# Performance work log

Hardware: AMD Instinct MI355X
Metric: run time of the kernel (lower is better)

Reference implementation:

```python
import jax, jax.numpy as jnp
import numpy as np

INPUT_SIZE = 695 + 2 * 406 + 84  # 1591
HIDDEN = 1024
NUM_LAYERS = 2
B, T = 8, 2048


def _make_linear(key, fan_in, fan_out, forget_bias):
    kw, kb = jax.random.split(key)
    bound = 1.0 / np.sqrt(fan_in)
    W = jax.random.uniform(kw, (fan_in, fan_out), minval=-bound, maxval=bound, dtype=jnp.float32)
    b = jax.random.uniform(kb, (fan_out,), minval=-bound, maxval=bound, dtype=jnp.float32)
    H = fan_out // 3
    b = b.at[H:2 * H].set(forget_bias)  # init_input_passthrough: forget-gate bias = 6.0
    return W, b


def setup_inputs() -> dict:
    key = jax.random.key(0)
    k1, k2, k3, k4, k5 = jax.random.split(key, 5)
    prev_actions = jax.random.uniform(k1, (B, T, 695), dtype=jnp.float32)
    states = jax.random.uniform(k2, (B, T, 812), dtype=jnp.float32)
    metadata = jax.random.uniform(k3, (B, T, 84), dtype=jnp.float32)
    W1, b1 = _make_linear(k4, INPUT_SIZE, 3 * HIDDEN, 6.0)
    W2, b2 = _make_linear(k5, HIDDEN, 3 * HIDDEN, 6.0)
    return {"prev_actions": prev_actions, "states": states, "metadata": metadata,
            "W1": W1, "b1": b1, "W2": W2, "b2": b2}


def forget_mult(f, z):
    # c_t = f_t * z_t + (1 - f_t) * c_{t-1}, c_0 = 0; parallel (log-depth) scan over time.
    a = 1.0 - f          # decay
    b = f * z            # input term
    def combine(c1, c2):
        a1, b1 = c1
        a2, b2 = c2
        return a1 * a2, a2 * b1 + b2
    _, c = jax.lax.associative_scan(combine, (a, b), axis=-2)
    return c


def qrnn_layer(x, W, b):
    y = jnp.einsum('btd,dh->bth', x, W) + b          # [B,T,3H]
    Z, Fg, O = jnp.split(y, 3, axis=-1)
    C = forget_mult(jax.nn.sigmoid(Fg), jax.nn.relu(Z))  # [B,T,H]
    out = jax.nn.sigmoid(O) * C
    return out, C[..., -1, :]


def reference(prev_actions, states, metadata, W1, b1, W2, b2):
    x = jnp.concatenate([prev_actions, states, metadata], axis=-1)  # [B,T,1591]
    hs = []
    for W, b in ((W1, b1), (W2, b2)):
        x, h_last = qrnn_layer(x, W, b)
        hs.append(h_last)
    h = jnp.stack(hs, axis=-2)  # [B, num_layers, H]
    return x, h
```

## Files before the change

### kernel.cpp

```cpp
#include <hip/hip_runtime.h>

typedef unsigned short u16;
typedef unsigned int   u32;
typedef __attribute__((ext_vector_type(8))) short bf16x8;
typedef __attribute__((ext_vector_type(4))) float f32x4;

#define B_ 8
#define T_ 2048
#define M_ 16384
#define N_ 3072
#define H_ 1024
#define L_ 64
#define NC_ 32

__device__ __forceinline__ u16 f2bf(float f) {
    union { float f; unsigned u; } v; v.f = f;
    unsigned r = v.u + 0x7FFFu + ((v.u >> 16) & 1u);
    return (u16)(r >> 16);
}
__device__ __forceinline__ float bf2f(u16 s) {
    union { unsigned u; float f; } v; v.u = ((unsigned)s) << 16;
    return v.f;
}
__device__ __forceinline__ float sigm(float x) {
    return 1.f / (1.f + __expf(-x));
}

__device__ __forceinline__ void gload_lds16(const void* g, void* l) {
    __builtin_amdgcn_global_load_lds(
        (const __attribute__((address_space(1))) unsigned int*)g,
        (__attribute__((address_space(3))) unsigned int*)l,
        16, 0, 0);
}

__global__ void concat_cast(const float* __restrict__ pa, const float* __restrict__ st,
                            const float* __restrict__ md, u16* __restrict__ x) {
    const int m = blockIdx.x;
    const float* pam = pa + (size_t)m * 695;
    const float* stm = st + (size_t)m * 812;
    const float* mdm = md + (size_t)m * 84;
    u16* xm = x + (size_t)m * 1600;
    for (int d = threadIdx.x; d < 1600; d += 256) {
        float v;
        if (d < 695)       v = pam[d];
        else if (d < 1507) v = stm[d - 695];
        else if (d < 1591) v = mdm[d - 1507];
        else               v = 0.f;
        xm[d] = f2bf(v);
    }
}

__global__ void wtrans(const float* __restrict__ W, u16* __restrict__ Wt, int K, int Kp) {
    __shared__ float tile[32][33];
    const int n0 = blockIdx.x << 5;
    const int k0 = blockIdx.y << 5;
    const int tx = threadIdx.x & 31, ty = threadIdx.x >> 5;
    #pragma unroll
    for (int i = 0; i < 32; i += 8) {
        int k = k0 + ty + i;
        tile[ty + i][tx] = (k < K) ? W[(size_t)k * N_ + n0 + tx] : 0.f;
    }
    __syncthreads();
    #pragma unroll
    for (int i = 0; i < 32; i += 8) {
        int n = n0 + ty + i;
        Wt[(size_t)n * Kp + k0 + tx] = f2bf(tile[tx][ty + i]);
    }
}

#define AO_(c, kh) ((((c) << 2) + (kh)) << 13)
#define BO_(c, kh) ((((c) << 2) + 2 + (kh)) << 13)

__global__ __launch_bounds__(512, 1)
void gemm8p(const u16* __restrict__ A, const u16* __restrict__ Bt,
            const float* __restrict__ bias, u16* __restrict__ Y,
            int Kp, int NK, int NBN) {
    __shared__ u16 lds[65536];
    const int tid = threadIdx.x;
    const int w = tid >> 6, l = tid & 63;
    const int wm = w >> 2, wn = w & 3;

    const int cpx = gridDim.x >> 3;
    const int xg = (blockIdx.x & 7) * cpx + (blockIdx.x >> 3);
    const int bm = xg / NBN, bn = xg % NBN;
    const int brow = bm << 8, bcol = bn << 8;

    const int srow = l >> 2;
    const int gslot = (l & 3) ^ (srow & 3);
    const u16* ga = A  + (size_t)(brow + w * 32 + srow) * Kp + gslot * 8;
    const u16* gb = Bt + (size_t)(bcol + w * 32 + srow) * Kp + gslot * 8;
    const int ldst = w << 10;

    const int fl = ((l & 15) << 5) + ((((l >> 4) ^ (l & 3)) & 3) << 3);
    const int abase0 = (wm << 7) << 5;
    const int bbase0 = (wn << 6) << 5;

#define STG(OFF, gp, kt, kh) do {                                              \
    gload_lds16((gp) + (size_t)(kt) * 64 + (kh) * 32, &lds[(OFF) + ldst]);     \
    gload_lds16((gp) + 16 * (size_t)Kp + (size_t)(kt) * 64 + (kh) * 32,        \
                &lds[(OFF) + ldst + 512]);                                     \
} while (0)

    f32x4 acc[8][4] = {};
    bf16x8 bfr[4];

    STG(AO_(0, 0), ga, 0, 0); STG(BO_(0, 0), gb, 0, 0);
    STG(AO_(0, 1), ga, 0, 1); STG(BO_(0, 1), gb, 0, 1);
    STG(AO_(1, 0), ga, 1, 0); STG(BO_(1, 0), gb, 1, 0);
    asm volatile("s_waitcnt vmcnt(4)" ::: "memory");
    __builtin_amdgcn_s_barrier();
    asm volatile("" ::: "memory");

#define PHASE(CH, KH, LOADB, STAGECODE, VMW) do {                              \
    bf16x8 af[4];                                                              \
    { const int ab = AO_(cur, KH) + abase0 + ((CH) << 11);                     \
      _Pragma("unroll")                                                        \
      for (int mf = 0; mf < 4; ++mf)                                           \
          af[mf] = *reinterpret_cast<const bf16x8*>(&lds[ab + (mf << 9) + fl]);\
    }                                                                          \
    if (LOADB) {                                                               \
        const int bb = BO_(cur, KH) + bbase0;                                  \
        _Pragma("unroll")                                                      \
        for (int nf = 0; nf < 4; ++nf)                                         \
            bfr[nf] = *reinterpret_cast<const bf16x8*>(&lds[bb + (nf << 9) + fl]); \
    }                                                                          \
    STAGECODE;                                                                 \
    if (VMW) asm volatile("s_waitcnt vmcnt(4)" ::: "memory");                  \
    asm volatile("" ::: "memory");                                             \
    __builtin_amdgcn_s_barrier();                                              \
    asm volatile("s_waitcnt lgkmcnt(0)" ::: "memory");                         \
    __builtin_amdgcn_sched_barrier(0);                                         \
    __builtin_amdgcn_s_setprio(1);                                             \
    _Pragma("unroll")                                                          \
    for (int mf = 0; mf < 4; ++mf)                                             \
        _Pragma("unroll")                                                      \
        for (int nf = 0; nf < 4; ++nf)                                         \
            acc[(CH) * 4 + mf][nf] = __builtin_amdgcn_mfma_f32_16x16x32_bf16(  \
                af[mf], bfr[nf], acc[(CH) * 4 + mf][nf], 0, 0, 0);             \
    __builtin_amdgcn_s_setprio(0);                                             \
    __builtin_amdgcn_sched_barrier(0);                                         \
    __builtin_amdgcn_s_barrier();                                              \
    asm volatile("" ::: "memory");                                             \
} while (0)

    for (int kt = 0; kt < NK; ++kt) {
        const int cur = kt & 1;
        const int kn1 = (kt + 1 < NK) ? kt + 1 : kt;
        const int kn2 = (kt + 2 < NK) ? kt + 2 : kt;
        PHASE(0, 0, 1, { STG(AO_(cur ^ 1, 1), ga, kn1, 1); }, 0);
        PHASE(1, 0, 0, { STG(BO_(cur ^ 1, 1), gb, kn1, 1); }, 1);
        PHASE(0, 1, 1, { STG(AO_(cur, 0),     ga, kn2, 0); }, 0);
        PHASE(1, 1, 0, { STG(BO_(cur, 0),     gb, kn2, 0); }, 1);
    }

    asm volatile("s_waitcnt vmcnt(0)" ::: "memory");

    const int crow0 = brow + wm * 128 + ((l >> 4) << 2);
    const int ccol0 = bcol + wn * 64 + (l & 15);
    #pragma unroll
    for (int nf = 0; nf < 4; ++nf) {
        const int gc = ccol0 + nf * 16;
        const float bv = bias[gc];
        #pragma unroll
        for (int mfi = 0; mfi < 8; ++mfi) {
            #pragma unroll
            for (int j = 0; j < 4; ++j)
                Y[(size_t)(crow0 + mfi * 16 + j) * N_ + gc] = f2bf(acc[mfi][nf][j] + bv);
        }
    }
#undef PHASE
#undef STG
}

__global__ void scan_p1(const u16* __restrict__ y, float* __restrict__ aprod,
                        float* __restrict__ cend) {
    const int hb = blockIdx.x & 1;
    const int chunk = (blockIdx.x >> 1) & (NC_ - 1);
    const int b = blockIdx.x >> 6;
    const int h = (hb << 9) + (threadIdx.x << 1);
    const u16* yb = y + ((size_t)b * T_ + (size_t)chunk * L_) * N_;
    float a0 = 1.f, a1 = 1.f, c0 = 0.f, c1 = 0.f;
    #pragma unroll 4
    for (int t = 0; t < L_; ++t) {
        const u32 zz = *reinterpret_cast<const u32*>(&yb[t * N_ + h]);
        const u32 ff = *reinterpret_cast<const u32*>(&yb[t * N_ + H_ + h]);
        const float f0 = sigm(bf2f((u16)ff));
        const float f1 = sigm(bf2f((u16)(ff >> 16)));
        const float z0 = fmaxf(bf2f((u16)zz), 0.f);
        const float z1 = fmaxf(bf2f((u16)(zz >> 16)), 0.f);
        c0 = f0 * z0 + (1.f - f0) * c0;  a0 *= (1.f - f0);
        c1 = f1 * z1 + (1.f - f1) * c1;  a1 *= (1.f - f1);
    }
    const size_t idx = ((size_t)b * NC_ + chunk) * H_ + h;
    *reinterpret_cast<float2*>(&aprod[idx]) = make_float2(a0, a1);
    *reinterpret_cast<float2*>(&cend[idx])  = make_float2(c0, c1);
}

__global__ void scan_p2(const float* __restrict__ aprod, const float* __restrict__ cend,
                        float* __restrict__ cin, float* __restrict__ hout, int layer) {
    const int b = blockIdx.x >> 2;
    const int h = ((blockIdx.x & 3) << 8) + threadIdx.x;
    float c = 0.f;
    #pragma unroll
    for (int k = 0; k < NC_; ++k) {
        const size_t idx = ((size_t)b * NC_ + k) * H_ + h;
        cin[idx] = c;
        c = aprod[idx] * c + cend[idx];
    }
    hout[(size_t)(((b << 1) + layer) << 10) + h] = c;
}

__global__ void scan_p3(const u16* __restrict__ y, const float* __restrict__ cin,
                        void* __restrict__ xout, int layer) {
    const int hb = blockIdx.x & 1;
    const int chunk = (blockIdx.x >> 1) & (NC_ - 1);
    const int b = blockIdx.x >> 6;
    const int h = (hb << 9) + (threadIdx.x << 1);
    const u16* yb = y + ((size_t)b * T_ + (size_t)chunk * L_) * N_;
    const size_t cidx = ((size_t)b * NC_ + chunk) * H_ + h;
    const float2 cv = *reinterpret_cast<const float2*>(&cin[cidx]);
    float c0 = cv.x, c1 = cv.y;
    u32*    xo_bf = (u32*)xout;
    float2* xo_f  = (float2*)xout;
    const size_t obase = ((size_t)b * T_ + (size_t)chunk * L_) * H_ + h;
    #pragma unroll 4
    for (int t = 0; t < L_; ++t) {
        const u32 zz = *reinterpret_cast<const u32*>(&yb[t * N_ + h]);
        const u32 ff = *reinterpret_cast<const u32*>(&yb[t * N_ + H_ + h]);
        const u32 oo = *reinterpret_cast<const u32*>(&yb[t * N_ + 2 * H_ + h]);
        const float f0 = sigm(bf2f((u16)ff));
        const float f1 = sigm(bf2f((u16)(ff >> 16)));
        const float z0 = fmaxf(bf2f((u16)zz), 0.f);
        const float z1 = fmaxf(bf2f((u16)(zz >> 16)), 0.f);
        c0 = f0 * z0 + (1.f - f0) * c0;
        c1 = f1 * z1 + (1.f - f1) * c1;
        const float o0 = sigm(bf2f((u16)oo)) * c0;
        const float o1 = sigm(bf2f((u16)(oo >> 16))) * c1;
        const size_t oi = obase + (size_t)t * H_;
        if (layer) xo_f[oi >> 1] = make_float2(o0, o1);
        else       xo_bf[oi >> 1] = (u32)f2bf(o0) | ((u32)f2bf(o1) << 16);
    }
}

extern "C" void kernel_launch(void* const* d_in, const int* in_sizes, int n_in,
                              void* d_out, int out_size, void* d_ws, size_t ws_size,
                              hipStream_t stream) {
    const float* pa = (const float*)d_in[0];
    const float* st = (const float*)d_in[1];
    const float* md = (const float*)d_in[2];
    const float* W1 = (const float*)d_in[3];
    const float* b1 = (const float*)d_in[4];
    const float* W2 = (const float*)d_in[5];
    const float* b2 = (const float*)d_in[6];
    float* out = (float*)d_out;

    char* ws = (char*)d_ws;
    const size_t y_bytes = (size_t)M_ * N_ * 2;
    const size_t x_bytes = (size_t)M_ * 1600 * 2;
    u16* y  = (u16*)ws;
    u16* x  = (u16*)(ws + y_bytes);
    u16* Wt = (u16*)(ws + y_bytes + x_bytes);
    char* scr = ws + y_bytes + (size_t)M_ * H_ * 2;
    const size_t sarr = (size_t)B_ * NC_ * H_ * 4;
    float* aprod = (float*)scr;
    float* cend  = (float*)(scr + sarr);
    float* cin   = (float*)(scr + 2 * sarr);

    float* hout = out + (size_t)M_ * H_;

    const int grid_g = (M_ / 256) * (N_ / 256);

    concat_cast<<<M_, 256, 0, stream>>>(pa, st, md, x);
    wtrans<<<dim3(N_ / 32, 50), 256, 0, stream>>>(W1, Wt, 1591, 1600);
    gemm8p<<<grid_g, 512, 0, stream>>>(x, Wt, b1, y, 1600, 25, N_ / 256);
    scan_p1<<<B_ * NC_ * 2, 256, 0, stream>>>(y, aprod, cend);
    scan_p2<<<32, 256, 0, stream>>>(aprod, cend, cin, hout, 0);
    scan_p3<<<B_ * NC_ * 2, 256, 0, stream>>>(y, cin, x, 0);

    wtrans<<<dim3(N_ / 32, 32), 256, 0, stream>>>(W2, Wt, 1024, 1024);
    gemm8p<<<grid_g, 512, 0, stream>>>(x, Wt, b2, y, 1024, 16, N_ / 256);
    scan_p1<<<B_ * NC_ * 2, 256, 0, stream>>>(y, aprod, cend);
    scan_p2<<<32, 256, 0, stream>>>(aprod, cend, cin, hout, 1);
    scan_p3<<<B_ * NC_ * 2, 256, 0, stream>>>(y, cin, out, 1);
}
```

Before: 455.1 us.

## Switch GEMM to 32x32x16 MFMA with 4-stage K=32 pipeline and vector stores

Replaces the 16x16x32 bf16 MFMA tiling with 32x32x16 instructions, so each wave holds 4x2 accumulator tiles of 16 floats. K tiles shrink to 32 and the LDS ring grows from double buffering to four stages, with one barrier per half-step instead of two. The epilogue now writes packed 8-byte bf16 stores with vectorised bias loads. The aims are fewer LDS fragment reads per FLOP, fewer barriers, and coalesced output stores, at the cost of more loop iterations and a new swizzle that must stay correct.

Measured after the change: 473.8 us. 4.1% more time.

```diff
diff --git a/kernel.cpp b/kernel.cpp
--- a/kernel.cpp
+++ b/kernel.cpp
@@ -3,7 +3,8 @@
 typedef unsigned short u16;
 typedef unsigned int   u32;
 typedef __attribute__((ext_vector_type(8))) short bf16x8;
-typedef __attribute__((ext_vector_type(4))) float f32x4;
+typedef __attribute__((ext_vector_type(16))) float f32x16;
+typedef __attribute__((ext_vector_type(2))) unsigned int u32x2;
 
 #define B_ 8
 #define T_ 2048
@@ -68,9 +69,6 @@
     }
 }
 
-#define AO_(c, kh) ((((c) << 2) + (kh)) << 13)
-#define BO_(c, kh) ((((c) << 2) + 2 + (kh)) << 13)
-
 __global__ __launch_bounds__(512, 1)
 void gemm8p(const u16* __restrict__ A, const u16* __restrict__ Bt,
             const float* __restrict__ bias, u16* __restrict__ Y,
@@ -85,91 +83,97 @@
     const int bm = xg / NBN, bn = xg % NBN;
     const int brow = bm << 8, bcol = bn << 8;
 
-    const int srow = l >> 2;
-    const int gslot = (l & 3) ^ (srow & 3);
-    const u16* ga = A  + (size_t)(brow + w * 32 + srow) * Kp + gslot * 8;
-    const u16* gb = Bt + (size_t)(bcol + w * 32 + srow) * Kp + gslot * 8;
+    const int srow = (w << 5) + (l >> 2);
+    const int gslot = (l & 3) ^ ((l >> 3) & 3);
+    const u16* ga = A  + (size_t)(brow + srow) * Kp + gslot * 8;
+    const u16* gb = Bt + (size_t)(bcol + srow) * Kp + gslot * 8;
     const int ldst = w << 10;
 
-    const int fl = ((l & 15) << 5) + ((((l >> 4) ^ (l & 3)) & 3) << 3);
-    const int abase0 = (wm << 7) << 5;
-    const int bbase0 = (wn << 6) << 5;
-
-#define STG(OFF, gp, kt, kh) do {                                              \
-    gload_lds16((gp) + (size_t)(kt) * 64 + (kh) * 32, &lds[(OFF) + ldst]);     \
-    gload_lds16((gp) + 16 * (size_t)Kp + (size_t)(kt) * 64 + (kh) * 32,        \
-                &lds[(OFF) + ldst + 512]);                                     \
+    const int flK = ((l & 31) << 5) + ((((l >> 5) ^ ((l >> 1) & 3)) & 3) << 3);
+    const int abase = wm << 12;
+    const int bbase = 8192 + (wn << 11);
+
+#define STG_A(r, kt) do {                                                      \
+    gload_lds16(ga + (size_t)(kt) * 32,                 &lds[((r) << 14) + ldst]);        \
+    gload_lds16(ga + (size_t)(kt) * 32 + 16 * (size_t)Kp, &lds[((r) << 14) + ldst + 512]); \
 } while (0)
-
-    f32x4 acc[8][4] = {};
-    bf16x8 bfr[4];
-
-    STG(AO_(0, 0), ga, 0, 0); STG(BO_(0, 0), gb, 0, 0);
-    STG(AO_(0, 1), ga, 0, 1); STG(BO_(0, 1), gb, 0, 1);
-    STG(AO_(1, 0), ga, 1, 0); STG(BO_(1, 0), gb, 1, 0);
-    asm volatile("s_waitcnt vmcnt(4)" ::: "memory");
+#define STG_B(r, kt) do {                                                      \
+    gload_lds16(gb + (size_t)(kt) * 32,                 &lds[((r) << 14) + 8192 + ldst]);        \
+    gload_lds16(gb + (size_t)(kt) * 32 + 16 * (size_t)Kp, &lds[((r) << 14) + 8192 + ldst + 512]); \
+} while (0)
+
+    f32x16 acc[4][2] = {};
+
+    STG_A(0, 0); STG_B(0, 0);
+    STG_A(1, 1); STG_B(1, 1);
+    STG_A(2, 2); STG_B(2, 2);
+    asm volatile("s_waitcnt vmcnt(8)" ::: "memory");
     __builtin_amdgcn_s_barrier();
     asm volatile("" ::: "memory");
 
-#define PHASE(CH, KH, LOADB, STAGECODE, VMW) do {                              \
-    bf16x8 af[4];                                                              \
-    { const int ab = AO_(cur, KH) + abase0 + ((CH) << 11);                     \
-      _Pragma("unroll")                                                        \
-      for (int mf = 0; mf < 4; ++mf)                                           \
-          af[mf] = *reinterpret_cast<const bf16x8*>(&lds[ab + (mf << 9) + fl]);\
-    }                                                                          \
-    if (LOADB) {                                                               \
-        const int bb = BO_(cur, KH) + bbase0;                                  \
-        _Pragma("unroll")                                                      \
-        for (int nf = 0; nf < 4; ++nf)                                         \
-            bfr[nf] = *reinterpret_cast<const bf16x8*>(&lds[bb + (nf << 9) + fl]); \
-    }                                                                          \
+#define PH(KH, STAGECODE, WAITCODE) do {                                       \
+    bf16x8 af[4], bfr[2];                                                      \
+    const int fl = flK ^ ((KH) << 4);                                          \
+    const int cb = cur << 14;                                                  \
+    _Pragma("unroll")                                                          \
+    for (int mi = 0; mi < 4; ++mi)                                             \
+        af[mi] = *reinterpret_cast<const bf16x8*>(&lds[cb + abase + (mi << 10) + fl]); \
+    _Pragma("unroll")                                                          \
+    for (int ni = 0; ni < 2; ++ni)                                             \
+        bfr[ni] = *reinterpret_cast<const bf16x8*>(&lds[cb + bbase + (ni << 10) + fl]); \
     STAGECODE;                                                                 \
-    if (VMW) asm volatile("s_waitcnt vmcnt(4)" ::: "memory");                  \
-    asm volatile("" ::: "memory");                                             \
+    WAITCODE;                                                                  \
     __builtin_amdgcn_s_barrier();                                              \
-    asm volatile("s_waitcnt lgkmcnt(0)" ::: "memory");                         \
     __builtin_amdgcn_sched_barrier(0);                                         \
     __builtin_amdgcn_s_setprio(1);                                             \
     _Pragma("unroll")                                                          \
-    for (int mf = 0; mf < 4; ++mf)                                             \
+    for (int mi = 0; mi < 4; ++mi)                                             \
         _Pragma("unroll")                                                      \
-        for (int nf = 0; nf < 4; ++nf)                                         \
-            acc[(CH) * 4 + mf][nf] = __builtin_amdgcn_mfma_f32_16x16x32_bf16(  \
-                af[mf], bfr[nf], acc[(CH) * 4 + mf][nf], 0, 0, 0);             \
+        for (int ni = 0; ni < 2; ++ni)                                         \
+            acc[mi][ni] = __builtin_amdgcn_mfma_f32_32x32x16_bf16(             \
+                bfr[ni], af[mi], acc[mi][ni], 0, 0, 0);                        \
     __builtin_amdgcn_s_setprio(0);                                             \
     __builtin_amdgcn_sched_barrier(0);                                         \
-    __builtin_amdgcn_s_barrier();                                              \
-    asm volatile("" ::: "memory");                                             \
 } while (0)
 
     for (int kt = 0; kt < NK; ++kt) {
-        const int cur = kt & 1;
-        const int kn1 = (kt + 1 < NK) ? kt + 1 : kt;
-        const int kn2 = (kt + 2 < NK) ? kt + 2 : kt;
-        PHASE(0, 0, 1, { STG(AO_(cur ^ 1, 1), ga, kn1, 1); }, 0);
-        PHASE(1, 0, 0, { STG(BO_(cur ^ 1, 1), gb, kn1, 1); }, 1);
-        PHASE(0, 1, 1, { STG(AO_(cur, 0),     ga, kn2, 0); }, 0);
-        PHASE(1, 1, 0, { STG(BO_(cur, 0),     gb, kn2, 0); }, 1);
-    }
-
+        const int cur = kt & 3;
+        const int nxt = (kt + 3 < NK) ? kt + 3 : kt;
+        const int nb = (kt + 3) & 3;
+        PH(0, { STG_A(nb, nxt); },
+              { asm volatile("s_waitcnt lgkmcnt(0)" ::: "memory"); });
+        PH(1, { STG_B(nb, nxt); },
+              { asm volatile("s_waitcnt vmcnt(8) lgkmcnt(0)" ::: "memory"); });
+    }
     asm volatile("s_waitcnt vmcnt(0)" ::: "memory");
 
-    const int crow0 = brow + wm * 128 + ((l >> 4) << 2);
-    const int ccol0 = bcol + wn * 64 + (l & 15);
-    #pragma unroll
-    for (int nf = 0; nf < 4; ++nf) {
-        const int gc = ccol0 + nf * 16;
-        const float bv = bias[gc];
+    const int m0 = brow + wm * 128 + (l & 31);
+    const int nlb = bcol + wn * 64 + ((l >> 5) << 2);
+    float4 bv[2][4];
+    #pragma unroll
+    for (int ni = 0; ni < 2; ++ni)
         #pragma unroll
-        for (int mfi = 0; mfi < 8; ++mfi) {
+        for (int q = 0; q < 4; ++q)
+            bv[ni][q] = *reinterpret_cast<const float4*>(&bias[nlb + ni * 32 + q * 8]);
+    #pragma unroll
+    for (int mi = 0; mi < 4; ++mi) {
+        u16* yrow = Y + (size_t)(m0 + mi * 32) * N_;
+        #pragma unroll
+        for (int ni = 0; ni < 2; ++ni) {
             #pragma unroll
-            for (int j = 0; j < 4; ++j)
-                Y[(size_t)(crow0 + mfi * 16 + j) * N_ + gc] = f2bf(acc[mfi][nf][j] + bv);
+            for (int q = 0; q < 4; ++q) {
+                u32x2 p;
+                p.x = (u32)f2bf(acc[mi][ni][q * 4 + 0] + bv[ni][q].x) |
+                      ((u32)f2bf(acc[mi][ni][q * 4 + 1] + bv[ni][q].y) << 16);
+                p.y = (u32)f2bf(acc[mi][ni][q * 4 + 2] + bv[ni][q].z) |
+                      ((u32)f2bf(acc[mi][ni][q * 4 + 3] + bv[ni][q].w) << 16);
+                *reinterpret_cast<u32x2*>(&yrow[nlb + ni * 32 + q * 8]) = p;
+            }
         }
     }
-#undef PHASE
-#undef STG
+#undef PH
+#undef STG_A
+#undef STG_B
 }
 
 __global__ void scan_p1(const u16* __restrict__ y, float* __restrict__ aprod,
@@ -272,13 +276,13 @@
 
     concat_cast<<<M_, 256, 0, stream>>>(pa, st, md, x);
     wtrans<<<dim3(N_ / 32, 50), 256, 0, stream>>>(W1, Wt, 1591, 1600);
-    gemm8p<<<grid_g, 512, 0, stream>>>(x, Wt, b1, y, 1600, 25, N_ / 256);
+    gemm8p<<<grid_g, 512, 0, stream>>>(x, Wt, b1, y, 1600, 50, N_ / 256);
     scan_p1<<<B_ * NC_ * 2, 256, 0, stream>>>(y, aprod, cend);
     scan_p2<<<32, 256, 0, stream>>>(aprod, cend, cin, hout, 0);
     scan_p3<<<B_ * NC_ * 2, 256, 0, stream>>>(y, cin, x, 0);
 
     wtrans<<<dim3(N_ / 32, 32), 256, 0, stream>>>(W2, Wt, 1024, 1024);
-    gemm8p<<<grid_g, 512, 0, stream>>>(x, Wt, b2, y, 1024, 16, N_ / 256);
+    gemm8p<<<grid_g, 512, 0, stream>>>(x, Wt, b2, y, 1024, 32, N_ / 256);
     scan_p1<<<B_ * NC_ * 2, 256, 0, stream>>>(y, aprod, cend);
     scan_p2<<<32, 256, 0, stream>>>(aprod, cend, cin, hout, 1);
     scan_p3<<<B_ * NC_ * 2, 256, 0, stream>>>(y, cin, out, 1);
```
